# Kernel tuning notes

Hardware: AMD Instinct MI355X
Metric: run time of the kernel (lower is better)

The kernel has to match this reference:

```python
import jax, jax.numpy as jnp
import numpy as np
import math

D_MODEL = 2048
N_HEADS = 32
N_KV_HEADS = 8
HEAD_DIM = D_MODEL // N_HEADS  # 64
N_GROUPS = N_HEADS // N_KV_HEADS  # 4
MAX_SEQ_LEN = 2048
ROPE_THETA = 500000.0


def precompute_rope(head_dim, max_seq_len, theta=ROPE_THETA):
    freqs = 1.0 / theta ** (jnp.arange(0, head_dim, 2, dtype=jnp.float32) / head_dim)
    positions = jnp.arange(max_seq_len, dtype=jnp.float32)
    angles = jnp.outer(positions, freqs)  # [S, head_dim/2]
    return jnp.cos(angles), jnp.sin(angles)


def apply_rope(x, cos, sin):
    # x: [B, H, S, D]; cos/sin: [S, D/2]
    half = x.shape[-1] // 2
    x1, x2 = x[..., :half], x[..., half:]
    cos = cos[None, None]
    sin = sin[None, None]
    return jnp.concatenate([x1 * cos - x2 * sin, x1 * sin + x2 * cos], axis=-1)


def setup_inputs() -> dict:
    key = jax.random.key(0)
    k1, k2, k3, k4, k5 = jax.random.split(key, 5)
    B, S = 2, 2048
    x = jax.random.normal(k1, (B, S, D_MODEL), dtype=jnp.float32)
    sd = 1.0 / math.sqrt(D_MODEL)
    # weights stored as [in, out] so forward is x @ W (same math as torch Linear)
    W_q = jax.random.normal(k2, (D_MODEL, N_HEADS * HEAD_DIM), dtype=jnp.float32) * sd
    W_k = jax.random.normal(k3, (D_MODEL, N_KV_HEADS * HEAD_DIM), dtype=jnp.float32) * sd
    W_v = jax.random.normal(k4, (D_MODEL, N_KV_HEADS * HEAD_DIM), dtype=jnp.float32) * sd
    W_o = jax.random.normal(k5, (N_HEADS * HEAD_DIM, D_MODEL), dtype=jnp.float32) * sd
    cos, sin = precompute_rope(HEAD_DIM, MAX_SEQ_LEN)
    return {"x": x, "W_q": W_q, "W_k": W_k, "W_v": W_v, "W_o": W_o,
            "rope_cos": cos, "rope_sin": sin}


def reference(x, W_q, W_k, W_v, W_o, rope_cos, rope_sin):
    B, S, _ = x.shape
    scale = 1.0 / math.sqrt(HEAD_DIM)
    # projections -> [B, H, S, D]
    q = (x @ W_q).reshape(B, S, N_HEADS, HEAD_DIM).transpose(0, 2, 1, 3)
    k = (x @ W_k).reshape(B, S, N_KV_HEADS, HEAD_DIM).transpose(0, 2, 1, 3)
    v = (x @ W_v).reshape(B, S, N_KV_HEADS, HEAD_DIM).transpose(0, 2, 1, 3)
    # RoPE
    q = apply_rope(q, rope_cos[:S], rope_sin[:S])
    k = apply_rope(k, rope_cos[:S], rope_sin[:S])
    # GQA expand: repeat each KV head n_groups times
    k = jnp.repeat(k, N_GROUPS, axis=1)  # [B, H, S, D]
    v = jnp.repeat(v, N_GROUPS, axis=1)
    # scores + causal mask + softmax
    scores = jnp.einsum('bhqd,bhkd->bhqk', q, k) * scale
    causal = jnp.tril(jnp.ones((S, S), dtype=bool))
    scores = jnp.where(causal[None, None], scores, -jnp.inf)
    weights = jax.nn.softmax(scores, axis=-1)
    attn_out = jnp.einsum('bhqk,bhkd->bhqd', weights, v)
    out = attn_out.transpose(0, 2, 1, 3).reshape(B, S, N_HEADS * HEAD_DIM) @ W_o
    return out
```

## Files before the change

### kernel.cpp

```cpp
#include <hip/hip_runtime.h>
#include <hip/hip_bf16.h>

typedef __attribute__((ext_vector_type(8))) short short8;
typedef __attribute__((ext_vector_type(4))) short short4v;
typedef __attribute__((ext_vector_type(4))) float f32x4;

#define MFMA(A,B,C) __builtin_amdgcn_mfma_f32_16x16x32_bf16(A,B,C,0,0,0)
#define SW(row) ((((row) & 3)) | (((row) >> 1) & 4))
#define SCL 0.18033688f

__device__ __forceinline__ short f2bs(float f) {
    __hip_bfloat16 h = __float2bfloat16(f);
    union { __hip_bfloat16 h; short s; } u; u.h = h; return u.s;
}

__device__ __forceinline__ float exp2v(float x) {
    float r; asm("v_exp_f32 %0, %1" : "=v"(r) : "v"(x)); return r;
}

__device__ __forceinline__ unsigned cvtpk(float a, float b) {
    unsigned r; asm("v_cvt_pk_bf16_f32 %0, %1, %2" : "=v"(r) : "v"(a), "v"(b)); return r;
}

__device__ __forceinline__ void async16(void* lds, const void* g) {
    __builtin_amdgcn_global_load_lds(
        (const __attribute__((address_space(1))) unsigned int*)g,
        (__attribute__((address_space(3))) unsigned int*)lds, 16, 0, 0);
}

__global__ __launch_bounds__(256) void prep_k(
    const float* __restrict__ x,
    const float* __restrict__ Wq, const float* __restrict__ Wk,
    const float* __restrict__ Wv, const float* __restrict__ Wo,
    short* __restrict__ x_bf, short* __restrict__ Wqkv_t, short* __restrict__ Wo_t)
{
    __shared__ float tile[32][33];
    int bid = blockIdx.x;
    const int t = threadIdx.x;

    if (bid < 8192) {
        int i = bid * 256 + t;
        const float4 v = *(const float4*)(x + (size_t)i * 4);
        short4v o;
        o.x = f2bs(v.x); o.y = f2bs(v.y); o.z = f2bs(v.z); o.w = f2bs(v.w);
        *(short4v*)(x_bf + (size_t)i * 4) = o;
        return;
    }
    bid -= 8192;

    const float* W; short* Wt; int nbx;
    const int K = 2048;
    if (bid < 4096)      { W = Wq; Wt = Wqkv_t;                          nbx = 64; }
    else if (bid < 5120) { bid -= 4096; W = Wk; Wt = Wqkv_t + (size_t)2048 * 2048; nbx = 16; }
    else if (bid < 6144) { bid -= 5120; W = Wv; Wt = Wqkv_t + (size_t)2560 * 2048; nbx = 16; }
    else                 { bid -= 6144; W = Wo; Wt = Wo_t;               nbx = 64; }
    const int N = nbx * 32;
    const int tx = t & 31, ty = t >> 5;
    const int n0 = (bid % nbx) * 32, k0 = (bid / nbx) * 32;

    #pragma unroll
    for (int i = 0; i < 32; i += 8)
        tile[ty + i][tx] = W[(size_t)(k0 + ty + i) * N + n0 + tx];
    __syncthreads();
    #pragma unroll
    for (int i = 0; i < 32; i += 8)
        Wt[(size_t)(n0 + ty + i) * K + k0 + tx] = f2bs(tile[tx][ty + i]);
}

__global__ __launch_bounds__(512, 2) void gemm_qkv_k(
    const short* __restrict__ A, const short* __restrict__ Bt,
    short* __restrict__ Cq, short* __restrict__ Ck, short* __restrict__ Cv,
    const float* __restrict__ rc, const float* __restrict__ rs,
    int M, int N, int K)
{
    extern __shared__ short lds[];
    const int t = threadIdx.x;
    const int l = t & 63, w = t >> 6;
    const int lo = l & 15, hi = l >> 4;
    const int wm = w >> 2, wn = w & 3;
    const int lr8 = l >> 3, ls8 = l & 7;

    const int nbx = gridDim.x;
    const int nwg = nbx * gridDim.y;
    const int bid0 = blockIdx.y * nbx + blockIdx.x;
    const int wg = (bid0 & 7) * (nwg >> 3) + (bid0 >> 3);
    const int tm = (wg % nbx) * 256, tn = (wg / nbx) * 256;

    const f32x4 z4 = {0.f, 0.f, 0.f, 0.f};
    f32x4 acc[8][4];
    #pragma unroll
    for (int m = 0; m < 8; ++m)
        #pragma unroll
        for (int n = 0; n < 4; ++n) acc[m][n] = z4;

    auto stageA = [&](int kt, int buf, int h) {
        const size_t ko = (size_t)kt * 64;
        const int rbase = h * 128;
        short* dst = lds + buf * 32768 + rbase * 64;
        #pragma unroll
        for (int j = 0; j < 2; ++j) {
            int g = w * 2 + j;
            int row = g * 8 + lr8;
            int gs = ls8 ^ SW(row);
            async16(dst + g * 512, A + (size_t)(tm + rbase + row) * K + ko + gs * 8);
        }
    };
    auto stageB = [&](int kt, int buf, int j) {
        const size_t ko = (size_t)kt * 64;
        short* dst = lds + buf * 32768 + 16384 + j * 4096 + w * 512;
        int row = j * 64 + w * 8 + lr8;
        int gs = ls8 ^ SW(row);
        async16(dst, Bt + (size_t)(tn + row) * K + ko + gs * 8);
    };
    auto stage_tile = [&](int kt, int buf) {
        stageA(kt, buf, 0);
        stageB(kt, buf, 0);
        stageA(kt, buf, 1);
        stageB(kt, buf, 1);
        stageB(kt, buf, 2);
        stageB(kt, buf, 3);
    };
    auto wave_wait = [&]() {
        switch (w) {
            case 0: asm volatile("s_waitcnt vmcnt(5)" ::: "memory"); break;
            case 1: asm volatile("s_waitcnt vmcnt(2)" ::: "memory"); break;
            case 2: asm volatile("s_waitcnt vmcnt(1)" ::: "memory"); break;
            case 3: asm volatile("s_waitcnt vmcnt(0)" ::: "memory"); break;
            case 4: asm volatile("s_waitcnt vmcnt(3)" ::: "memory"); break;
            case 5: asm volatile("s_waitcnt vmcnt(2)" ::: "memory"); break;
            case 6: asm volatile("s_waitcnt vmcnt(1)" ::: "memory"); break;
            default: asm volatile("s_waitcnt vmcnt(0)" ::: "memory"); break;
        }
    };

    const int nkt = K >> 6;
    stage_tile(0, 0);
    wave_wait();
    __builtin_amdgcn_s_barrier();

    int cur = 0;
    for (int kt = 0; kt < nkt; ++kt) {
        const bool pf = (kt + 1 < nkt);
        if (pf) stage_tile(kt + 1, cur ^ 1);
        const short* Ab_ = lds + cur * 32768;
        const short* Bb_ = Ab_ + 16384;

        __builtin_amdgcn_s_setprio(1);
        #pragma unroll
        for (int ks = 0; ks < 2; ++ks) {
            const int slot = ks * 4 + hi;
            short8 bfr[4];
            #pragma unroll
            for (int n = 0; n < 4; ++n) {
                int row = wn * 64 + n * 16 + lo;
                bfr[n] = *(const short8*)(Bb_ + row * 64 + ((slot ^ SW(row)) << 3));
            }
            #pragma unroll
            for (int mh = 0; mh < 2; ++mh) {
                short8 af[4];
                #pragma unroll
                for (int mm = 0; mm < 4; ++mm) {
                    int row = wm * 128 + (mh * 4 + mm) * 16 + lo;
                    af[mm] = *(const short8*)(Ab_ + row * 64 + ((slot ^ SW(row)) << 3));
                }
                #pragma unroll
                for (int n = 0; n < 4; ++n)
                    #pragma unroll
                    for (int mm = 0; mm < 4; ++mm)
                        acc[mh * 4 + mm][n] = MFMA(af[mm], bfr[n], acc[mh * 4 + mm][n]);
            }
        }
        __builtin_amdgcn_s_setprio(0);

        if (pf) {
            wave_wait();
            __builtin_amdgcn_s_barrier();
        }
        cur ^= 1;
    }

    const int ctn = tn + wn * 64;
    if (ctn < 2048) {
        #pragma unroll
        for (int m = 0; m < 8; ++m)
            #pragma unroll
            for (int r = 0; r < 4; ++r) {
                int row = tm + wm * 128 + m * 16 + hi * 4 + r;
                int b = row >> 11, s = row & 2047;
                #pragma unroll
                for (int n = 0; n < 2; ++n) {
                    int col = ctn + n * 16 + lo;
                    int h = col >> 6, d = col & 63;
                    float x1 = acc[m][n][r], x2 = acc[m][n + 2][r];
                    float c = rc[s * 32 + d], sn = rs[s * 32 + d];
                    size_t base = (((size_t)b * 32 + h) * 2048 + s) * 64;
                    Cq[base + d]      = f2bs((x1 * c - x2 * sn) * SCL);
                    Cq[base + d + 32] = f2bs((x1 * sn + x2 * c) * SCL);
                }
            }
    } else if (ctn < 2560) {
        #pragma unroll
        for (int m = 0; m < 8; ++m)
            #pragma unroll
            for (int r = 0; r < 4; ++r) {
                int row = tm + wm * 128 + m * 16 + hi * 4 + r;
                int b = row >> 11, s = row & 2047;
                #pragma unroll
                for (int n = 0; n < 2; ++n) {
                    int col = ctn - 2048 + n * 16 + lo;
                    int h = col >> 6, d = col & 63;
                    float x1 = acc[m][n][r], x2 = acc[m][n + 2][r];
                    float c = rc[s * 32 + d], sn = rs[s * 32 + d];
                    size_t base = (((size_t)b * 8 + h) * 2048 + s) * 64;
                    Ck[base + d]      = f2bs(x1 * c - x2 * sn);
                    Ck[base + d + 32] = f2bs(x1 * sn + x2 * c);
                }
            }
    } else {
        #pragma unroll
        for (int m = 0; m < 8; ++m)
            #pragma unroll
            for (int r = 0; r < 4; ++r) {
                int row = tm + wm * 128 + m * 16 + hi * 4 + r;
                int b = row >> 11, s = row & 2047;
                #pragma unroll
                for (int n = 0; n < 4; ++n) {
                    int col = ctn - 2560 + n * 16 + lo;
                    int h = col >> 6, d = col & 63;
                    Cv[(((size_t)b * 8 + h) * 64 + d) * 2048 + s] = f2bs(acc[m][n][r]);
                }
            }
    }
}

__global__ __launch_bounds__(512, 2) void gemm_o_k(
    const short* __restrict__ A, const short* __restrict__ Bt,
    float* __restrict__ Cf, int M, int N, int K)
{
    extern __shared__ short lds[];
    const int t = threadIdx.x;
    const int l = t & 63, w = t >> 6;
    const int lo = l & 15, hi = l >> 4;
    const int wm = w >> 2, wn = w & 3;
    const int lr = l >> 3, ls = l & 7;

    const int nbx = gridDim.x;
    const int nwg = nbx * gridDim.y;
    const int bid0 = blockIdx.y * nbx + blockIdx.x;
    const int wg = (bid0 & 7) * (nwg >> 3) + (bid0 >> 3);
    const int tm = (wg % nbx) * 128, tn = (wg / nbx) * 256;

    const f32x4 z4 = {0.f, 0.f, 0.f, 0.f};
    f32x4 acc[4][4];
    #pragma unroll
    for (int m = 0; m < 4; ++m)
        #pragma unroll
        for (int n = 0; n < 4; ++n) acc[m][n] = z4;

    const int srow = w * 8 + lr;
    const int sswz = ls ^ SW(srow);

    auto stage_unit = [&](int kt, int buf, int u) {
        const size_t ko = (size_t)kt * 64;
        short* base = lds + buf * 24576;
        if (u < 2)
            async16(base + u * 4096 + w * 512,
                    A + (size_t)(tm + u * 64 + srow) * K + ko + sswz * 8);
        else
            async16(base + 8192 + (u - 2) * 4096 + w * 512,
                    Bt + (size_t)(tn + (u - 2) * 64 + srow) * K + ko + sswz * 8);
    };

    const int nkt = K >> 6;
    #pragma unroll
    for (int u = 0; u < 6; ++u) stage_unit(0, 0, u);
    #pragma unroll
    for (int u = 0; u < 6; ++u) stage_unit(1, 1, u);
    asm volatile("s_waitcnt vmcnt(6)" ::: "memory");
    __builtin_amdgcn_s_barrier();

    int cur = 0;
    for (int kt = 0; kt < nkt; ++kt) {
        int tgt = cur + 2; if (tgt >= 3) tgt -= 3;
        const bool pf2 = (kt + 2 < nkt);
        const bool pf1 = (kt + 1 < nkt);
        const short* Ab_ = lds + cur * 24576;
        const short* Bb_ = Ab_ + 8192;
        short8 af[4], bfr[4];
        #pragma unroll
        for (int ph = 0; ph < 2; ++ph) {
            const int slot = ph * 4 + hi;
            #pragma unroll
            for (int mm = 0; mm < 4; ++mm) {
                int row = wm * 64 + mm * 16 + lo;
                af[mm] = *(const short8*)(Ab_ + row * 64 + ((slot ^ SW(row)) << 3));
            }
            #pragma unroll
            for (int n = 0; n < 4; ++n) {
                int row = wn * 64 + n * 16 + lo;
                bfr[n] = *(const short8*)(Bb_ + row * 64 + ((slot ^ SW(row)) << 3));
            }
            if (pf2) {
                stage_unit(kt + 2, tgt, ph * 3);
                stage_unit(kt + 2, tgt, ph * 3 + 1);
                stage_unit(kt + 2, tgt, ph * 3 + 2);
            }
            __builtin_amdgcn_s_barrier();
            asm volatile("s_waitcnt lgkmcnt(0)" ::: "memory");
            __builtin_amdgcn_sched_barrier(0);
            __builtin_amdgcn_s_setprio(1);
            #pragma unroll
            for (int n = 0; n < 4; ++n)
                #pragma unroll
                for (int mm = 0; mm < 4; ++mm)
                    acc[mm][n] = MFMA(af[mm], bfr[n], acc[mm][n]);
            __builtin_amdgcn_s_setprio(0);
            if (ph == 1) {
                if (pf2)      asm volatile("s_waitcnt vmcnt(6)" ::: "memory");
                else if (pf1) asm volatile("s_waitcnt vmcnt(0)" ::: "memory");
            }
            __builtin_amdgcn_s_barrier();
        }
        cur = (cur == 2) ? 0 : cur + 1;
    }

    #pragma unroll
    for (int m = 0; m < 4; ++m)
        #pragma unroll
        for (int r = 0; r < 4; ++r) {
            int row = tm + wm * 64 + m * 16 + hi * 4 + r;
            #pragma unroll
            for (int n = 0; n < 4; ++n) {
                int col = tn + wn * 64 + n * 16 + lo;
                Cf[(size_t)row * N + col] = acc[m][n][r];
            }
        }
}

__global__ __launch_bounds__(256) void attn_k(
    const short* __restrict__ Qp, const short* __restrict__ Kp, const short* __restrict__ Vt,
    short* __restrict__ Ab)
{
    __shared__ short KV[2][8192];
    const int t = threadIdx.x, l = t & 63, w = t >> 6;
    const int lo = l & 15, hi = l >> 4;
    const int lr = l >> 3, ls = l & 7;
    const int pair = blockIdx.x;
    const int h = blockIdx.y, b = blockIdx.z;
    const int kvh = h >> 2;
    const size_t qbase  = (size_t)(b * 32 + h) * 2048 * 64;
    const size_t kbase  = (size_t)(b * 8 + kvh) * 2048 * 64;
    const size_t vtbase = (size_t)(b * 8 + kvh) * 64 * 2048;
    const size_t abase  = (size_t)b * 2048 * 2048 + (size_t)h * 64;

    for (int halfq = 0; halfq < 2; ++halfq) {
        const int qtile = halfq ? 31 - pair : pair;
        const int nkt = qtile + 1;

        short8 qf[2];
        {
            int qrow = qtile * 64 + w * 16 + lo;
            #pragma unroll
            for (int ks = 0; ks < 2; ++ks)
                qf[ks] = *(const short8*)(Qp + qbase + (size_t)qrow * 64 + (ks * 4 + hi) * 8);
        }

        const f32x4 z4 = {0.f, 0.f, 0.f, 0.f};
        float l_run = 0.f;
        f32x4 oacc[4];
        #pragma unroll
        for (int nd = 0; nd < 4; ++nd) oacc[nd] = z4;

        #pragma unroll
        for (int j = 0; j < 2; ++j) {
            int g8 = w * 2 + j;
            int row = g8 * 8 + lr;
            int gs = ls ^ SW(row);
            async16(&KV[0][g8 * 512],        Kp + kbase + (size_t)row * 64 + gs * 8);
            async16(&KV[0][4096 + g8 * 512], Vt + vtbase + (size_t)row * 2048 + gs * 8);
        }
        __syncthreads();

        int cur = 0;
        for (int kt = 0; kt < nkt; ++kt) {
            if (kt + 1 < nkt) {
                #pragma unroll
                for (int j = 0; j < 2; ++j) {
                    int g8 = w * 2 + j;
                    int row = g8 * 8 + lr;
                    int gs = ls ^ SW(row);
                    async16(&KV[cur ^ 1][g8 * 512],
                            Kp + kbase + (size_t)((kt + 1) * 64 + row) * 64 + gs * 8);
                    async16(&KV[cur ^ 1][4096 + g8 * 512],
                            Vt + vtbase + (size_t)row * 2048 + (kt + 1) * 64 + gs * 8);
                }
            }

            const short* Ks = &KV[cur][0];
            const short* Vs = &KV[cur][4096];

            f32x4 sacc[4];
            #pragma unroll
            for (int n = 0; n < 4; ++n) sacc[n] = z4;
            __builtin_amdgcn_s_setprio(1);
            #pragma unroll
            for (int ks = 0; ks < 2; ++ks) {
                const int slot = ks * 4 + hi;
                #pragma unroll
                for (int n = 0; n < 4; ++n) {
                    const int krow = ((lo >> 2) << 3) + ((n & 1) << 2) + (lo & 3) + ((n >> 1) << 5);
                    short8 kf = *(const short8*)(Ks + krow * 64 + ((slot ^ SW(krow)) << 3));
                    sacc[n] = MFMA(kf, qf[ks], sacc[n]);
                }
            }
            __builtin_amdgcn_s_setprio(0);

            float p[4][4];
            if (kt == qtile) {
                const int q = qtile * 64 + w * 16 + lo;
                #pragma unroll
                for (int n = 0; n < 4; ++n)
                    #pragma unroll
                    for (int r = 0; r < 4; ++r) {
                        int k = kt * 64 + hi * 8 + ((n & 1) << 2) + r + ((n >> 1) << 5);
                        p[n][r] = exp2v((k > q) ? -3e38f : sacc[n][r]);
                    }
            } else {
                #pragma unroll
                for (int n = 0; n < 4; ++n)
                    #pragma unroll
                    for (int r = 0; r < 4; ++r)
                        p[n][r] = exp2v(sacc[n][r]);
            }
            float rs0 = 0.f, rs1 = 0.f;
            #pragma unroll
            for (int n = 0; n < 4; ++n) {
                rs0 += p[n][0] + p[n][1];
                rs1 += p[n][2] + p[n][3];
            }
            l_run += rs0 + rs1;

            short8 afr[2];
            #pragma unroll
            for (int ks = 0; ks < 2; ++ks) {
                union { short8 s; unsigned u[4]; } pk;
                pk.u[0] = cvtpk(p[2 * ks][0],     p[2 * ks][1]);
                pk.u[1] = cvtpk(p[2 * ks][2],     p[2 * ks][3]);
                pk.u[2] = cvtpk(p[2 * ks + 1][0], p[2 * ks + 1][1]);
                pk.u[3] = cvtpk(p[2 * ks + 1][2], p[2 * ks + 1][3]);
                afr[ks] = pk.s;
            }

            __builtin_amdgcn_s_setprio(1);
            #pragma unroll
            for (int ks = 0; ks < 2; ++ks) {
                const int slot = ks * 4 + hi;
                #pragma unroll
                for (int nd = 0; nd < 4; ++nd) {
                    const int vrow = nd * 16 + lo;
                    short8 vf = *(const short8*)(Vs + vrow * 64 + ((slot ^ SW(vrow)) << 3));
                    oacc[nd] = MFMA(afr[ks], vf, oacc[nd]);
                }
            }
            __builtin_amdgcn_s_setprio(0);

            __syncthreads();
            cur ^= 1;
        }

        l_run += __shfl_xor(l_run, 16, 64);
        l_run += __shfl_xor(l_run, 32, 64);
        float rl[4];
        #pragma unroll
        for (int r = 0; r < 4; ++r)
            rl[r] = 1.0f / __shfl(l_run, (l & 48) | (hi * 4 + r), 64);
        #pragma unroll
        for (int nd = 0; nd < 4; ++nd)
            #pragma unroll
            for (int r = 0; r < 4; ++r) {
                int s = qtile * 64 + w * 16 + hi * 4 + r;
                Ab[abase + (size_t)s * 2048 + nd * 16 + lo] = f2bs(oacc[nd][r] * rl[r]);
            }
    }
}

extern "C" void kernel_launch(void* const* d_in, const int* in_sizes, int n_in,
                              void* d_out, int out_size, void* d_ws, size_t ws_size,
                              hipStream_t stream)
{
    const float* x  = (const float*)d_in[0];
    const float* Wq = (const float*)d_in[1];
    const float* Wk = (const float*)d_in[2];
    const float* Wv = (const float*)d_in[3];
    const float* Wo = (const float*)d_in[4];
    const float* rc = (const float*)d_in[5];
    const float* rs = (const float*)d_in[6];
    float* out = (float*)d_out;
    char* ws = (char*)d_ws;

    size_t off = 0;
    short* x_bf   = (short*)(ws + off); off += (size_t)4096 * 2048 * 2;
    short* Wqkv_t = (short*)(ws + off); off += (size_t)3072 * 2048 * 2;
    short* Wo_t   = (short*)(ws + off); off += (size_t)2048 * 2048 * 2;
    short* Qp     = (short*)(ws + off); off += (size_t)2 * 32 * 2048 * 64 * 2;
    short* Kp     = (short*)(ws + off); off += (size_t)2 * 8 * 2048 * 64 * 2;
    short* Vtb    = (short*)(ws + off); off += (size_t)2 * 8 * 64 * 2048 * 2;
    short* Ab     = (short*)(ws + off); off += (size_t)4096 * 2048 * 2;
    if (off > ws_size) return;

    const int LDS_QKV = 2 * 32768 * 2;
    const int LDS_O   = 3 * 24576 * 2;
    (void)hipFuncSetAttribute((const void*)gemm_qkv_k,
                              hipFuncAttributeMaxDynamicSharedMemorySize, LDS_QKV);
    (void)hipFuncSetAttribute((const void*)gemm_o_k,
                              hipFuncAttributeMaxDynamicSharedMemorySize, LDS_O);

    prep_k<<<18432, 256, 0, stream>>>(x, Wq, Wk, Wv, Wo, x_bf, Wqkv_t, Wo_t);

    gemm_qkv_k<<<dim3(16, 12), 512, LDS_QKV, stream>>>(x_bf, Wqkv_t, Qp, Kp, Vtb,
                                                       rc, rs, 4096, 3072, 2048);

    attn_k<<<dim3(16, 32, 2), 256, 0, stream>>>(Qp, Kp, Vtb, Ab);

    gemm_o_k<<<dim3(32, 8), 512, LDS_O, stream>>>(Ab, Wo_t, out, 4096, 2048, 2048);
}
```

Baseline: 169.4 us.

## Load QKV GEMM B operand directly into registers, bypassing LDS

In the QKV projection GEMM, the weight (B) tile is no longer staged through LDS. Each wave now loads its B fragments straight from global memory into registers, double-buffered across the two k-substeps, with one set prefetched for the next tile. Only the A tile stays in LDS, which halves the dynamic LDS allocation and removes the per-wave vmcnt staggering that B staging needed. The trade-off is uncoalesced 16-byte-per-lane global loads, B data fetched redundantly by waves that share columns, and higher register pressure.

After: 185.5 us. +9.5%, slower.

```diff
diff --git a/kernel.cpp b/kernel.cpp
--- a/kernel.cpp
+++ b/kernel.cpp
@@ -96,7 +96,7 @@
     auto stageA = [&](int kt, int buf, int h) {
         const size_t ko = (size_t)kt * 64;
         const int rbase = h * 128;
-        short* dst = lds + buf * 32768 + rbase * 64;
+        short* dst = lds + buf * 16384 + rbase * 64;
         #pragma unroll
         for (int j = 0; j < 2; ++j) {
             int g = w * 2 + j;
@@ -105,75 +105,70 @@
             async16(dst + g * 512, A + (size_t)(tm + rbase + row) * K + ko + gs * 8);
         }
     };
-    auto stageB = [&](int kt, int buf, int j) {
-        const size_t ko = (size_t)kt * 64;
-        short* dst = lds + buf * 32768 + 16384 + j * 4096 + w * 512;
-        int row = j * 64 + w * 8 + lr8;
-        int gs = ls8 ^ SW(row);
-        async16(dst, Bt + (size_t)(tn + row) * K + ko + gs * 8);
+    auto loadBks = [&](int kt, int ks, short8 (&B)[4]) {
+        #pragma unroll
+        for (int n = 0; n < 4; ++n) {
+            int row = tn + wn * 64 + n * 16 + lo;
+            B[n] = *(const short8*)(Bt + (size_t)row * K + kt * 64 + (ks * 4 + hi) * 8);
+        }
     };
-    auto stage_tile = [&](int kt, int buf) {
-        stageA(kt, buf, 0);
-        stageB(kt, buf, 0);
-        stageA(kt, buf, 1);
-        stageB(kt, buf, 1);
-        stageB(kt, buf, 2);
-        stageB(kt, buf, 3);
-    };
-    auto wave_wait = [&]() {
-        switch (w) {
-            case 0: asm volatile("s_waitcnt vmcnt(5)" ::: "memory"); break;
-            case 1: asm volatile("s_waitcnt vmcnt(2)" ::: "memory"); break;
-            case 2: asm volatile("s_waitcnt vmcnt(1)" ::: "memory"); break;
-            case 3: asm volatile("s_waitcnt vmcnt(0)" ::: "memory"); break;
-            case 4: asm volatile("s_waitcnt vmcnt(3)" ::: "memory"); break;
-            case 5: asm volatile("s_waitcnt vmcnt(2)" ::: "memory"); break;
-            case 6: asm volatile("s_waitcnt vmcnt(1)" ::: "memory"); break;
-            default: asm volatile("s_waitcnt vmcnt(0)" ::: "memory"); break;
-        }
-    };
 
     const int nkt = K >> 6;
-    stage_tile(0, 0);
-    wave_wait();
+    short8 Ba[4], Bb[4];
+
+    stageA(0, 0, 0); stageA(0, 0, 1);
+    loadBks(0, 0, Ba);
+    asm volatile("" ::: "memory");
+    asm volatile("s_waitcnt vmcnt(4)" ::: "memory");
     __builtin_amdgcn_s_barrier();
 
     int cur = 0;
     for (int kt = 0; kt < nkt; ++kt) {
         const bool pf = (kt + 1 < nkt);
-        if (pf) stage_tile(kt + 1, cur ^ 1);
-        const short* Ab_ = lds + cur * 32768;
-        const short* Bb_ = Ab_ + 16384;
-
+        if (pf) { stageA(kt + 1, cur ^ 1, 0); stageA(kt + 1, cur ^ 1, 1); }
+        const short* Ab_ = lds + cur * 16384;
+
+        loadBks(kt, 1, Bb);
+        asm volatile("" ::: "memory");
         __builtin_amdgcn_s_setprio(1);
         #pragma unroll
-        for (int ks = 0; ks < 2; ++ks) {
-            const int slot = ks * 4 + hi;
-            short8 bfr[4];
-            #pragma unroll
-            for (int n = 0; n < 4; ++n) {
-                int row = wn * 64 + n * 16 + lo;
-                bfr[n] = *(const short8*)(Bb_ + row * 64 + ((slot ^ SW(row)) << 3));
-            }
-            #pragma unroll
-            for (int mh = 0; mh < 2; ++mh) {
-                short8 af[4];
-                #pragma unroll
-                for (int mm = 0; mm < 4; ++mm) {
-                    int row = wm * 128 + (mh * 4 + mm) * 16 + lo;
-                    af[mm] = *(const short8*)(Ab_ + row * 64 + ((slot ^ SW(row)) << 3));
-                }
-                #pragma unroll
-                for (int n = 0; n < 4; ++n)
-                    #pragma unroll
-                    for (int mm = 0; mm < 4; ++mm)
-                        acc[mh * 4 + mm][n] = MFMA(af[mm], bfr[n], acc[mh * 4 + mm][n]);
-            }
+        for (int mh = 0; mh < 2; ++mh) {
+            short8 af[4];
+            #pragma unroll
+            for (int mm = 0; mm < 4; ++mm) {
+                int row = wm * 128 + (mh * 4 + mm) * 16 + lo;
+                af[mm] = *(const short8*)(Ab_ + row * 64 + ((hi ^ SW(row)) << 3));
+            }
+            #pragma unroll
+            for (int n = 0; n < 4; ++n)
+                #pragma unroll
+                for (int mm = 0; mm < 4; ++mm)
+                    acc[mh * 4 + mm][n] = MFMA(af[mm], Ba[n], acc[mh * 4 + mm][n]);
         }
         __builtin_amdgcn_s_setprio(0);
 
+        if (pf) loadBks(kt + 1, 0, Ba);
+        asm volatile("" ::: "memory");
+        __builtin_amdgcn_s_setprio(1);
+        #pragma unroll
+        for (int mh = 0; mh < 2; ++mh) {
+            short8 af[4];
+            #pragma unroll
+            for (int mm = 0; mm < 4; ++mm) {
+                int row = wm * 128 + (mh * 4 + mm) * 16 + lo;
+                int slot = 4 + hi;
+                af[mm] = *(const short8*)(Ab_ + row * 64 + ((slot ^ SW(row)) << 3));
+            }
+            #pragma unroll
+            for (int n = 0; n < 4; ++n)
+                #pragma unroll
+                for (int mm = 0; mm < 4; ++mm)
+                    acc[mh * 4 + mm][n] = MFMA(af[mm], Bb[n], acc[mh * 4 + mm][n]);
+        }
+        __builtin_amdgcn_s_setprio(0);
+
         if (pf) {
-            wave_wait();
+            asm volatile("s_waitcnt vmcnt(8)" ::: "memory");
             __builtin_amdgcn_s_barrier();
         }
         cur ^= 1;
@@ -508,7 +503,7 @@
     short* Ab     = (short*)(ws + off); off += (size_t)4096 * 2048 * 2;
     if (off > ws_size) return;
 
-    const int LDS_QKV = 2 * 32768 * 2;
+    const int LDS_QKV = 2 * 16384 * 2;
     const int LDS_O   = 3 * 24576 * 2;
     (void)hipFuncSetAttribute((const void*)gemm_qkv_k,
                               hipFuncAttributeMaxDynamicSharedMemorySize, LDS_QKV);
```
